# Optimization experiments

Measured on AMD Instinct MI355X. Metric: run time of the kernel, lower is better.

Reference implementation:

```python
import jax, jax.numpy as jnp
import numpy as np

B, S, E, H, D = 4, 2048, 1024, 16, 64


def setup_inputs() -> dict:
    key = jax.random.key(0)
    ks = jax.random.split(key, 6)
    scale_in = 1.0 / np.sqrt(E)
    return {
        "x": jax.random.normal(ks[0], (B, S, E), dtype=jnp.float32),
        "Wq": jax.random.normal(ks[1], (H, E, D), dtype=jnp.float32) * scale_in,
        "bq": jnp.zeros((H, D), dtype=jnp.float32),
        "Wk": jax.random.normal(ks[2], (H, E, D), dtype=jnp.float32) * scale_in,
        "bk": jnp.zeros((H, D), dtype=jnp.float32),
        "Wv": jax.random.normal(ks[3], (H, E, D), dtype=jnp.float32) * scale_in,
        "bv": jnp.zeros((H, D), dtype=jnp.float32),
        "Wo": jax.random.normal(ks[4], (H * D, E), dtype=jnp.float32) * (1.0 / np.sqrt(H * D)),
        "bo": jnp.zeros((E,), dtype=jnp.float32),
    }


def reference(x, Wq, bq, Wk, bk, Wv, bv, Wo, bo):
    # Per-head Q/K/V projections, batched over heads: [B,S,E] x [H,E,D] -> [B,H,S,D]
    q = jnp.einsum("bse,hed->bhsd", x, Wq) + bq[None, :, None, :]
    k = jnp.einsum("bse,hed->bhsd", x, Wk) + bk[None, :, None, :]
    v = jnp.einsum("bse,hed->bhsd", x, Wv) + bv[None, :, None, :]

    d = q.shape[-1]
    scores = jnp.einsum("bhqd,bhkd->bhqk", q, k) / jnp.sqrt(jnp.asarray(d, q.dtype))
    # Causal mask (registered tril buffer of size max_seq_len in HeadAttention)
    seq = scores.shape[-1]
    causal = jnp.tril(jnp.ones((seq, seq), dtype=bool))
    scores = jnp.where(causal[None, None, :, :], scores, jnp.asarray(-1e9, scores.dtype))
    attn = jax.nn.softmax(scores, axis=-1)
    out = jnp.einsum("bhqk,bhkd->bhqd", attn, v)  # [B,H,S,D]

    # Concat heads: [B,S,H*D], then output projection (dropout is identity in eval)
    out = out.transpose(0, 2, 1, 3).reshape(out.shape[0], out.shape[2], -1)
    return out @ Wo + bo
```

## Files before the change

### kernel.cpp

```cpp
#include <hip/hip_runtime.h>

typedef __bf16 bf16x8 __attribute__((ext_vector_type(8)));
typedef __bf16 bf16x4 __attribute__((ext_vector_type(4)));
typedef float  f32x4  __attribute__((ext_vector_type(4)));

#define B_    4
#define S_    2048
#define E_    1024
#define H_    16
#define D_    64
#define MROWS (B_*S_)
#define HD3   3072

#define SCORE_SCALE 0.18033688011112043f

__device__ __forceinline__ void load_lds16(const void* g, void* l) {
  __builtin_amdgcn_global_load_lds((__attribute__((address_space(1))) void*)g,
                                   (__attribute__((address_space(3))) void*)l,
                                   16, 0, 0);
}

__device__ __forceinline__ f32x4 mfma16(bf16x8 a, bf16x8 b, f32x4 c) {
  return __builtin_amdgcn_mfma_f32_16x16x32_bf16(a, b, c, 0, 0, 0);
}

__device__ __forceinline__ int swz(int row, int dchunk) {
  return row * 64 + ((dchunk ^ (row & 7)) * 8);
}


__global__ void prep(const float4* __restrict__ x, const float* __restrict__ Wq,
                     const float* __restrict__ Wk, const float* __restrict__ Wv,
                     const float* __restrict__ bq, const float* __restrict__ bk,
                     const float* __restrict__ bv, const float* __restrict__ Wo,
                     __bf16* __restrict__ xb, __bf16* __restrict__ Wt,
                     float* __restrict__ bqkv, __bf16* __restrict__ Wot) {
  __shared__ float t[64][65];
  int bid = blockIdx.x;
  if (bid < 8192) {
    int id = bid * 256 + threadIdx.x;
    float4 v = x[id];
    bf16x4 o = { (__bf16)v.x, (__bf16)v.y, (__bf16)v.z, (__bf16)v.w };
    *(bf16x4*)(xb + 4 * (size_t)id) = o;
    return;
  }
  int tx = threadIdx.x & 63;
  int ty = threadIdx.x >> 6;
  if (bid < 8960) {
    int b2 = bid - 8192;
    int e0 = (b2 & 15) * 64;
    int h  = (b2 >> 4) & 15;
    int p  = b2 >> 8;
    const float* W    = (p == 0) ? Wq : (p == 1) ? Wk : Wv;
    const float* bsrc = (p == 0) ? bq : (p == 1) ? bk : bv;
#pragma unroll
    for (int r = 0; r < 16; ++r) {
      int eL = ty + r * 4;
      t[eL][tx] = W[((size_t)h * 1024 + (e0 + eL)) * 64 + tx];
    }
    __syncthreads();
#pragma unroll
    for (int r = 0; r < 16; ++r) {
      int d = ty + r * 4;
      Wt[((size_t)(p * 1024 + h * 64 + d)) * 1024 + e0 + tx] = (__bf16)t[tx][d];
    }
    if ((b2 & 15) == 0 && threadIdx.x < 64)
      bqkv[p * 1024 + h * 64 + threadIdx.x] = bsrc[h * 64 + threadIdx.x];
  } else {
    int b2 = bid - 8960;
    int hd0 = (b2 >> 4) * 64;
    int e0  = (b2 & 15) * 64;
#pragma unroll
    for (int r = 0; r < 16; ++r) {
      int hdL = ty + r * 4;
      t[hdL][tx] = Wo[(size_t)(hd0 + hdL) * 1024 + e0 + tx];
    }
    __syncthreads();
#pragma unroll
    for (int r = 0; r < 16; ++r) {
      int eL = ty + r * 4;
      Wot[(size_t)(e0 + eL) * 1024 + hd0 + tx] = (__bf16)t[tx][eL];
    }
  }
}


template <int MODE>
__global__ __launch_bounds__(256) void gemm_bt(const __bf16* __restrict__ A,
                                               const __bf16* __restrict__ Bt,
                                               const float* __restrict__ bias,
                                               void* __restrict__ Cout,
                                               __bf16* __restrict__ VT,
                                               int M, int N, int K) {
  __shared__ __attribute__((aligned(16))) __bf16 As[128 * 64];
  __shared__ __attribute__((aligned(16))) __bf16 Bs[128 * 64];
  int tid = threadIdx.x, wave = tid >> 6, lane = tid & 63;
  int quad = lane >> 4, cc = lane & 15;
  int nb = N >> 7;
  int bm = (int)blockIdx.x / nb, bn = (int)blockIdx.x % nb;
  const __bf16* Abase = A + (size_t)bm * 128 * K;
  const __bf16* Bbase = Bt + (size_t)bn * 128 * K;
  int wr = (wave >> 1) * 64, wc = (wave & 1) * 64;
  f32x4 acc[4][4];
#pragma unroll
  for (int i = 0; i < 4; ++i)
#pragma unroll
    for (int j = 0; j < 4; ++j) acc[i][j] = (f32x4){0.f, 0.f, 0.f, 0.f};

  int srow[4], scol[4];
#pragma unroll
  for (int p = 0; p < 4; ++p) {
    int g = tid + p * 256;
    srow[p] = g >> 3;
    scol[p] = ((g & 7) ^ (srow[p] & 7)) * 8;
  }
#pragma unroll
  for (int p = 0; p < 4; ++p) {
    load_lds16(Abase + (size_t)srow[p] * K + scol[p], &As[(tid + p * 256) * 8]);
    load_lds16(Bbase + (size_t)srow[p] * K + scol[p], &Bs[(tid + p * 256) * 8]);
  }

  for (int k0 = 0; k0 < K; k0 += 64) {
    __syncthreads();
    bf16x8 af[2][4], bf[2][4];
#pragma unroll
    for (int kk = 0; kk < 2; ++kk) {
#pragma unroll
      for (int i = 0; i < 4; ++i) af[kk][i] = *(const bf16x8*)&As[swz(wr + i * 16 + cc, kk * 4 + quad)];
#pragma unroll
      for (int j = 0; j < 4; ++j) bf[kk][j] = *(const bf16x8*)&Bs[swz(wc + j * 16 + cc, kk * 4 + quad)];
    }
    __syncthreads();
    if (k0 + 64 < K) {
      int kn = k0 + 64;
#pragma unroll
      for (int p = 0; p < 4; ++p) {
        load_lds16(Abase + (size_t)srow[p] * K + kn + scol[p], &As[(tid + p * 256) * 8]);
        load_lds16(Bbase + (size_t)srow[p] * K + kn + scol[p], &Bs[(tid + p * 256) * 8]);
      }
    }
#pragma unroll
    for (int kk = 0; kk < 2; ++kk)
#pragma unroll
      for (int i = 0; i < 4; ++i)
#pragma unroll
        for (int j = 0; j < 4; ++j) acc[kk ? i : i][j] = mfma16(af[kk][i], bf[kk][j], acc[i][j]);
  }

#pragma unroll
  for (int j = 0; j < 4; ++j) {
    int col = bn * 128 + wc + j * 16 + cc;
    float bv = bias[col];
#pragma unroll
    for (int i = 0; i < 4; ++i) {
      int row0 = bm * 128 + wr + i * 16 + quad * 4;
      if (MODE == 0) {
#pragma unroll
        for (int r = 0; r < 4; ++r)
          ((float*)Cout)[(size_t)(row0 + r) * N + col] = acc[i][j][r] + bv;
      } else if (col < 2048) {
        float sc = (col < 1024) ? SCORE_SCALE : 1.0f;
#pragma unroll
        for (int r = 0; r < 4; ++r)
          ((__bf16*)Cout)[(size_t)(row0 + r) * 2048 + col] = (__bf16)((acc[i][j][r] + bv) * sc);
      } else {
        int bh = (row0 >> 11) * 16 + ((col >> 6) & 15);
        int d  = col & 63;
        bf16x4 pk;
#pragma unroll
        for (int r = 0; r < 4; ++r) pk[r] = (__bf16)(acc[i][j][r] + bv);
        *(bf16x4*)&VT[((size_t)(bh * 64 + d)) * 2048 + (row0 & 2047)] = pk;
      }
    }
  }
}


__global__ __launch_bounds__(512, 4) void attn(const __bf16* __restrict__ QKb,
                                               const __bf16* __restrict__ VT,
                                               __bf16* __restrict__ O) {
  int bx = blockIdx.x;
  int bh = bx & 63;
  int qt = (bx < 256) ? (7 - (bx >> 6)) : ((bx >> 6) - 4);
  int h  = bh & 15;
  int b  = bh >> 4;
  int q0 = qt * 256;
  int tid = threadIdx.x, wave = tid >> 6, lane = tid & 63;
  int quad = lane >> 4, c = lane & 15;

  __shared__ __attribute__((aligned(16))) __bf16 smem[32768];
  __bf16* Qs = smem;
  __bf16* Ks = smem + 16384;
  __bf16* Vs = smem + 24576;
  __bf16* Ps = smem + wave * 2048;

  const __bf16* Qbase = QKb + (size_t)(b * S_ + q0) * 2048 + h * 64;
  const __bf16* Vbase = VT + (size_t)bh * (64 * 2048);
#pragma unroll
  for (int p = 0; p < 4; ++p) {
    int g = tid + p * 512;
    int row = g >> 3, pch = g & 7;
    load_lds16(Qbase + (size_t)row * 2048 + (pch ^ (row & 7)) * 8, &Qs[g * 8]);
  }
  {
    const __bf16* Kb = QKb + (size_t)(b * S_) * 2048 + 1024 + h * 64;
    int row = tid >> 3, pch = tid & 7;
    load_lds16(Kb + (size_t)row * 2048 + (pch ^ (row & 7)) * 8, &Ks[tid * 8]);
    load_lds16(Vbase + (size_t)row * 2048 + (pch ^ (row & 7)) * 8, &Vs[tid * 8]);
  }
  __syncthreads();

  bf16x8 qf[2][2];
#pragma unroll
  for (int i = 0; i < 2; ++i)
#pragma unroll
    for (int kk = 0; kk < 2; ++kk)
      qf[i][kk] = *(const bf16x8*)&Qs[swz(wave * 32 + i * 16 + c, kk * 4 + quad)];

  const __bf16 one_b = (__bf16)1.0f;
  bf16x8 ones = { one_b, one_b, one_b, one_b, one_b, one_b, one_b, one_b };

  f32x4 acc_o[2][4], acc_l[2];
#pragma unroll
  for (int i = 0; i < 2; ++i) {
    acc_l[i] = (f32x4){0.f, 0.f, 0.f, 0.f};
#pragma unroll
    for (int j = 0; j < 4; ++j) acc_o[i][j] = (f32x4){0.f, 0.f, 0.f, 0.f};
  }

  int qwave = q0 + wave * 32;
  int ntiles = qt * 4 + 4;
  for (int t = 0; t < ntiles; ++t) {
    int cur = t & 1;
    if (t + 1 < ntiles) {
      int kv1 = (t + 1) * 64;
      const __bf16* Kb = QKb + (size_t)(b * S_ + kv1) * 2048 + 1024 + h * 64;
      const __bf16* Vb = Vbase + kv1;
      int row = tid >> 3, pch = tid & 7;
      load_lds16(Kb + (size_t)row * 2048 + (pch ^ (row & 7)) * 8,
                 &Ks[(cur ^ 1) * 4096 + tid * 8]);
      load_lds16(Vb + (size_t)row * 2048 + (pch ^ (row & 7)) * 8,
                 &Vs[(cur ^ 1) * 4096 + tid * 8]);
    }

    int kv0 = t * 64;
    if (kv0 <= qwave + 31) {
      const __bf16* Kc = Ks + cur * 4096;
      const __bf16* Vc = Vs + cur * 4096;

      f32x4 acc_t[2][4];
#pragma unroll
      for (int i = 0; i < 2; ++i)
#pragma unroll
        for (int j = 0; j < 4; ++j) acc_t[i][j] = (f32x4){0.f, 0.f, 0.f, 0.f};
      bf16x8 kf[4][2];
#pragma unroll
      for (int j = 0; j < 4; ++j)
#pragma unroll
        for (int kk = 0; kk < 2; ++kk)
          kf[j][kk] = *(const bf16x8*)&Kc[swz(j * 16 + c, kk * 4 + quad)];
#pragma unroll
      for (int i = 0; i < 2; ++i)
#pragma unroll
        for (int j = 0; j < 4; ++j)
#pragma unroll
          for (int kk = 0; kk < 2; ++kk)
            acc_t[i][j] = mfma16(kf[j][kk], qf[i][kk], acc_t[i][j]);

      bool domask = (kv0 + 63 > qwave);
#pragma unroll
      for (int i = 0; i < 2; ++i) {
        int q_l = i * 16 + c;
        int q_g = qwave + q_l;
#pragma unroll
        for (int j = 0; j < 4; ++j) {
          bf16x4 pk;
#pragma unroll
          for (int r = 0; r < 4; ++r) {
            float p = __builtin_amdgcn_exp2f(acc_t[i][j][r]);
            if (domask) {
              int kv = kv0 + j * 16 + quad * 4 + r;
              p = (kv > q_g) ? 0.f : p;
            }
            pk[r] = (__bf16)p;
          }
          int dch8 = j * 2 + (quad >> 1);
          int phys = q_l * 64 + ((dch8 ^ (q_l & 7)) * 8) + (quad & 1) * 4;
          *(bf16x4*)&Ps[phys] = pk;
        }
      }

      bf16x8 pf[2][2], vf[4][2];
#pragma unroll
      for (int i = 0; i < 2; ++i)
#pragma unroll
        for (int kk = 0; kk < 2; ++kk)
          pf[i][kk] = *(const bf16x8*)&Ps[swz(i * 16 + c, kk * 4 + quad)];
#pragma unroll
      for (int j = 0; j < 4; ++j)
#pragma unroll
        for (int kk = 0; kk < 2; ++kk)
          vf[j][kk] = *(const bf16x8*)&Vc[swz(j * 16 + c, kk * 4 + quad)];
#pragma unroll
      for (int i = 0; i < 2; ++i) {
#pragma unroll
        for (int j = 0; j < 4; ++j)
#pragma unroll
          for (int kk = 0; kk < 2; ++kk)
            acc_o[i][j] = mfma16(pf[i][kk], vf[j][kk], acc_o[i][j]);
        acc_l[i] = mfma16(pf[i][0], ones, acc_l[i]);
        acc_l[i] = mfma16(pf[i][1], ones, acc_l[i]);
      }
    }

    __syncthreads();
  }

  __bf16* Obase = O + (size_t)(b * S_ + q0) * 1024 + h * 64;
#pragma unroll
  for (int i = 0; i < 2; ++i)
#pragma unroll
    for (int r = 0; r < 4; ++r) {
      float rl = 1.0f / acc_l[i][r];
      int row = wave * 32 + i * 16 + quad * 4 + r;
#pragma unroll
      for (int j = 0; j < 4; ++j)
        Obase[(size_t)row * 1024 + j * 16 + c] = (__bf16)(acc_o[i][j][r] * rl);
    }
}


extern "C" void kernel_launch(void* const* d_in, const int* in_sizes, int n_in,
                              void* d_out, int out_size, void* d_ws, size_t ws_size,
                              hipStream_t stream) {
  (void)in_sizes; (void)n_in; (void)out_size; (void)ws_size;
  const float* x  = (const float*)d_in[0];
  const float* Wq = (const float*)d_in[1];
  const float* bq = (const float*)d_in[2];
  const float* Wk = (const float*)d_in[3];
  const float* bk = (const float*)d_in[4];
  const float* Wv = (const float*)d_in[5];
  const float* bv = (const float*)d_in[6];
  const float* Wo = (const float*)d_in[7];
  const float* bo = (const float*)d_in[8];

  char* w = (char*)d_ws;
  __bf16* xb   = (__bf16*)(w);
  __bf16* Wt   = (__bf16*)(w + (16ull << 20));
  __bf16* Wot  = (__bf16*)(w + (22ull << 20));
  float*  bqkv = (float*) (w + (24ull << 20));
  __bf16* QKb  = (__bf16*)(w + (25ull << 20));
  __bf16* Ob   = (__bf16*)(w + (57ull << 20));
  __bf16* VT   = (__bf16*)(w + (73ull << 20));

  prep   <<<9216, 256, 0, stream>>>((const float4*)x, Wq, Wk, Wv, bq, bk, bv, Wo,
                                    xb, Wt, bqkv, Wot);
  gemm_bt<1><<<dim3((MROWS / 128) * (3072 / 128)), 256, 0, stream>>>(xb, Wt, bqkv, (void*)QKb, VT, MROWS, 3072, 1024);
  attn   <<<512, 512, 0, stream>>>(QKb, VT, Ob);
  gemm_bt<0><<<dim3((MROWS / 128) * (1024 / 128)), 256, 0, stream>>>(Ob, Wot, bo, d_out, nullptr, MROWS, 1024, 1024);
}
```

Before: 232.0 us.

## Split longest causal attention query tiles across two blocks and merge partials

The two heaviest query-tile groups (qt 6 and 7) are now each processed by two blocks that take alternating KV tiles. Each block writes unnormalized fp32 partial outputs and row sums to workspace, and a new merge kernel adds them and normalizes. The block order is reshuffled to balance load across the 640-block grid, and swizzle offsets are precomputed outside the loop. The aim is to shrink the causal tail imbalance, at the cost of an extra launch and extra fp32 workspace traffic. Because no running max is kept, the plain sum of partials is exact. PartO reuses the xb workspace region, which is no longer needed once the QKV GEMM has finished.

Measured after the change: 252.6 us. +8.9%, slower.

```diff
diff --git a/kernel.cpp b/kernel.cpp
--- a/kernel.cpp
+++ b/kernel.cpp
@@ -144,7 +144,7 @@
 #pragma unroll
       for (int i = 0; i < 4; ++i)
 #pragma unroll
-        for (int j = 0; j < 4; ++j) acc[kk ? i : i][j] = mfma16(af[kk][i], bf[kk][j], acc[i][j]);
+        for (int j = 0; j < 4; ++j) acc[i][j] = mfma16(af[kk][i], bf[kk][j], acc[i][j]);
   }
 
 #pragma unroll
@@ -178,15 +178,31 @@
 
 __global__ __launch_bounds__(512, 4) void attn(const __bf16* __restrict__ QKb,
                                                const __bf16* __restrict__ VT,
-                                               __bf16* __restrict__ O) {
+                                               __bf16* __restrict__ O,
+                                               float* __restrict__ PartO,
+                                               float* __restrict__ PartL) {
   int bx = blockIdx.x;
   int bh = bx & 63;
-  int qt = (bx < 256) ? (7 - (bx >> 6)) : ((bx >> 6) - 4);
+  int g  = bx >> 6;
+  int qt, par = 0, split = 0;
+  switch (g) {
+    case 0: qt = 5; break;
+    case 1: qt = 4; break;
+    case 2: qt = 7; split = 1; break;
+    case 3: qt = 7; par = 1; split = 1; break;
+    case 4: qt = 3; break;
+    case 5: qt = 6; split = 1; break;
+    case 6: qt = 6; par = 1; split = 1; break;
+    case 7: qt = 2; break;
+    case 8: qt = 1; break;
+    default: qt = 0; break;
+  }
   int h  = bh & 15;
   int b  = bh >> 4;
   int q0 = qt * 256;
   int tid = threadIdx.x, wave = tid >> 6, lane = tid & 63;
   int quad = lane >> 4, c = lane & 15;
+  int tstep = split ? 2 : 1;
 
   __shared__ __attribute__((aligned(16))) __bf16 smem[32768];
   __bf16* Qs = smem;
@@ -194,20 +210,23 @@
   __bf16* Vs = smem + 24576;
   __bf16* Ps = smem + wave * 2048;
 
+  int srow = tid >> 3, sx = ((tid & 7) ^ (srow & 7)) * 8;
+  const __bf16* Kp = QKb + ((size_t)(b * S_ + par * 64 + srow)) * 2048 + 1024 + h * 64 + sx;
+  const __bf16* Vp = VT + (size_t)bh * (64 * 2048) + (size_t)srow * 2048 + par * 64 + sx;
+  const int kstep = tstep * 64 * 2048;
+  const int vstep = tstep * 64;
+  int ldst = tid * 8;
+
   const __bf16* Qbase = QKb + (size_t)(b * S_ + q0) * 2048 + h * 64;
-  const __bf16* Vbase = VT + (size_t)bh * (64 * 2048);
 #pragma unroll
   for (int p = 0; p < 4; ++p) {
-    int g = tid + p * 512;
-    int row = g >> 3, pch = g & 7;
-    load_lds16(Qbase + (size_t)row * 2048 + (pch ^ (row & 7)) * 8, &Qs[g * 8]);
-  }
-  {
-    const __bf16* Kb = QKb + (size_t)(b * S_) * 2048 + 1024 + h * 64;
-    int row = tid >> 3, pch = tid & 7;
-    load_lds16(Kb + (size_t)row * 2048 + (pch ^ (row & 7)) * 8, &Ks[tid * 8]);
-    load_lds16(Vbase + (size_t)row * 2048 + (pch ^ (row & 7)) * 8, &Vs[tid * 8]);
-  }
+    int gg = tid + p * 512;
+    int row = gg >> 3, pch = gg & 7;
+    load_lds16(Qbase + (size_t)row * 2048 + (pch ^ (row & 7)) * 8, &Qs[gg * 8]);
+  }
+  load_lds16(Kp, &Ks[ldst]);
+  load_lds16(Vp, &Vs[ldst]);
+  Kp += kstep; Vp += vstep;
   __syncthreads();
 
   bf16x8 qf[2][2];
@@ -217,6 +236,21 @@
     for (int kk = 0; kk < 2; ++kk)
       qf[i][kk] = *(const bf16x8*)&Qs[swz(wave * 32 + i * 16 + c, kk * 4 + quad)];
 
+  int offA[4][2], offW[2][4];
+#pragma unroll
+  for (int j = 0; j < 4; ++j)
+#pragma unroll
+    for (int kk = 0; kk < 2; ++kk) offA[j][kk] = swz(j * 16 + c, kk * 4 + quad);
+#pragma unroll
+  for (int i = 0; i < 2; ++i) {
+    int q_l = i * 16 + c;
+#pragma unroll
+    for (int j = 0; j < 4; ++j) {
+      int dch8 = j * 2 + (quad >> 1);
+      offW[i][j] = q_l * 64 + ((dch8 ^ (q_l & 7)) * 8) + (quad & 1) * 4;
+    }
+  }
+
   const __bf16 one_b = (__bf16)1.0f;
   bf16x8 ones = { one_b, one_b, one_b, one_b, one_b, one_b, one_b, one_b };
 
@@ -230,17 +264,12 @@
 
   int qwave = q0 + wave * 32;
   int ntiles = qt * 4 + 4;
-  for (int t = 0; t < ntiles; ++t) {
-    int cur = t & 1;
-    if (t + 1 < ntiles) {
-      int kv1 = (t + 1) * 64;
-      const __bf16* Kb = QKb + (size_t)(b * S_ + kv1) * 2048 + 1024 + h * 64;
-      const __bf16* Vb = Vbase + kv1;
-      int row = tid >> 3, pch = tid & 7;
-      load_lds16(Kb + (size_t)row * 2048 + (pch ^ (row & 7)) * 8,
-                 &Ks[(cur ^ 1) * 4096 + tid * 8]);
-      load_lds16(Vb + (size_t)row * 2048 + (pch ^ (row & 7)) * 8,
-                 &Vs[(cur ^ 1) * 4096 + tid * 8]);
+  int cur = 0;
+  for (int t = par; t < ntiles; t += tstep) {
+    if (t + tstep < ntiles) {
+      load_lds16(Kp, &Ks[(cur ^ 1) * 4096 + ldst]);
+      load_lds16(Vp, &Vs[(cur ^ 1) * 4096 + ldst]);
+      Kp += kstep; Vp += vstep;
     }
 
     int kv0 = t * 64;
@@ -258,7 +287,7 @@
       for (int j = 0; j < 4; ++j)
 #pragma unroll
         for (int kk = 0; kk < 2; ++kk)
-          kf[j][kk] = *(const bf16x8*)&Kc[swz(j * 16 + c, kk * 4 + quad)];
+          kf[j][kk] = *(const bf16x8*)&Kc[offA[j][kk]];
 #pragma unroll
       for (int i = 0; i < 2; ++i)
 #pragma unroll
@@ -270,8 +299,7 @@
       bool domask = (kv0 + 63 > qwave);
 #pragma unroll
       for (int i = 0; i < 2; ++i) {
-        int q_l = i * 16 + c;
-        int q_g = qwave + q_l;
+        int q_g = qwave + i * 16 + c;
 #pragma unroll
         for (int j = 0; j < 4; ++j) {
           bf16x4 pk;
@@ -284,9 +312,7 @@
             }
             pk[r] = (__bf16)p;
           }
-          int dch8 = j * 2 + (quad >> 1);
-          int phys = q_l * 64 + ((dch8 ^ (q_l & 7)) * 8) + (quad & 1) * 4;
-          *(bf16x4*)&Ps[phys] = pk;
+          *(bf16x4*)&Ps[offW[i][j]] = pk;
         }
       }
 
@@ -295,12 +321,12 @@
       for (int i = 0; i < 2; ++i)
 #pragma unroll
         for (int kk = 0; kk < 2; ++kk)
-          pf[i][kk] = *(const bf16x8*)&Ps[swz(i * 16 + c, kk * 4 + quad)];
+          pf[i][kk] = *(const bf16x8*)&Ps[offA[i][kk]];
 #pragma unroll
       for (int j = 0; j < 4; ++j)
 #pragma unroll
         for (int kk = 0; kk < 2; ++kk)
-          vf[j][kk] = *(const bf16x8*)&Vc[swz(j * 16 + c, kk * 4 + quad)];
+          vf[j][kk] = *(const bf16x8*)&Vc[offA[j][kk]];
 #pragma unroll
       for (int i = 0; i < 2; ++i) {
 #pragma unroll
@@ -314,19 +340,63 @@
     }
 
     __syncthreads();
-  }
-
-  __bf16* Obase = O + (size_t)(b * S_ + q0) * 1024 + h * 64;
-#pragma unroll
-  for (int i = 0; i < 2; ++i)
-#pragma unroll
-    for (int r = 0; r < 4; ++r) {
-      float rl = 1.0f / acc_l[i][r];
-      int row = wave * 32 + i * 16 + quad * 4 + r;
-#pragma unroll
-      for (int j = 0; j < 4; ++j)
-        Obase[(size_t)row * 1024 + j * 16 + c] = (__bf16)(acc_o[i][j][r] * rl);
-    }
+    cur ^= 1;
+  }
+
+  if (!split) {
+    __bf16* Obase = O + (size_t)(b * S_ + q0) * 1024 + h * 64;
+#pragma unroll
+    for (int i = 0; i < 2; ++i)
+#pragma unroll
+      for (int r = 0; r < 4; ++r) {
+        float rl = 1.0f / acc_l[i][r];
+        int row = wave * 32 + i * 16 + quad * 4 + r;
+#pragma unroll
+        for (int j = 0; j < 4; ++j)
+          Obase[(size_t)row * 1024 + j * 16 + c] = (__bf16)(acc_o[i][j][r] * rl);
+      }
+  } else {
+    int slot = par * 128 + (7 - qt) * 64 + bh;
+    float* PO = PartO + (size_t)slot * (256 * 64);
+    float* PL = PartL + (size_t)slot * 256;
+#pragma unroll
+    for (int i = 0; i < 2; ++i)
+#pragma unroll
+      for (int r = 0; r < 4; ++r) {
+        int row = wave * 32 + i * 16 + quad * 4 + r;
+        if (c == 0) PL[row] = acc_l[i][r];
+#pragma unroll
+        for (int j = 0; j < 4; ++j)
+          PO[row * 64 + j * 16 + c] = acc_o[i][j][r];
+      }
+  }
+}
+
+__global__ void merge(const float* __restrict__ PartO, const float* __restrict__ PartL,
+                      __bf16* __restrict__ O) {
+  int u  = blockIdx.x >> 2;
+  int r0 = (blockIdx.x & 3) * 64;
+  int qt = 7 - (u >> 6);
+  int bh = u & 63;
+  int b = bh >> 4, h = bh & 15;
+  int q0 = qt * 256;
+  int tid = threadIdx.x;
+  const float* A0 = PartO + (size_t)u * (256 * 64) + r0 * 64;
+  const float* A1 = PartO + (size_t)(128 + u) * (256 * 64) + r0 * 64;
+  const float* L0 = PartL + (size_t)u * 256 + r0;
+  const float* L1 = PartL + (size_t)(128 + u) * 256 + r0;
+#pragma unroll
+  for (int it = 0; it < 4; ++it) {
+    int e = it * 1024 + tid * 4;
+    int row = e >> 6, d = e & 63;
+    f32x4 a0 = *(const f32x4*)&A0[e];
+    f32x4 a1 = *(const f32x4*)&A1[e];
+    float rl = 1.0f / (L0[row] + L1[row]);
+    bf16x4 o;
+#pragma unroll
+    for (int k = 0; k < 4; ++k) o[k] = (__bf16)((a0[k] + a1[k]) * rl);
+    *(bf16x4*)&O[(size_t)(b * S_ + q0 + r0 + row) * 1024 + h * 64 + d] = o;
+  }
 }
 
 
@@ -352,10 +422,13 @@
   __bf16* QKb  = (__bf16*)(w + (25ull << 20));
   __bf16* Ob   = (__bf16*)(w + (57ull << 20));
   __bf16* VT   = (__bf16*)(w + (73ull << 20));
+  float* PartO = (float*)(w);
+  float* PartL = (float*)(w + (18ull << 20));
 
   prep   <<<9216, 256, 0, stream>>>((const float4*)x, Wq, Wk, Wv, bq, bk, bv, Wo,
                                     xb, Wt, bqkv, Wot);
   gemm_bt<1><<<dim3((MROWS / 128) * (3072 / 128)), 256, 0, stream>>>(xb, Wt, bqkv, (void*)QKb, VT, MROWS, 3072, 1024);
-  attn   <<<512, 512, 0, stream>>>(QKb, VT, Ob);
+  attn   <<<640, 512, 0, stream>>>(QKb, VT, Ob, PartO, PartL);
+  merge  <<<512, 256, 0, stream>>>(PartO, PartL, Ob);
   gemm_bt<0><<<dim3((MROWS / 128) * (1024 / 128)), 256, 0, stream>>>(Ob, Wot, bo, d_out, nullptr, MROWS, 1024, 1024);
 }
```
